# Performance work log

Measured on AMD Instinct MI355X. Metric: run time of the kernel, lower is better.

Reference implementation:

```python
import jax, jax.numpy as jnp
import numpy as np

D_MODEL = 2048
NUM_HEADS = 16
D_K = D_MODEL // NUM_HEADS
THETA = 10000.0
MAX_SEQ_LEN = 2048
GPT_INIT_STD = 0.02


def setup_inputs() -> dict:
    key = jax.random.key(0)
    ks = jax.random.split(key, 5)
    B, T = 4, 2048
    x = jax.random.normal(ks[0], (B, T, D_MODEL), dtype=jnp.float32)
    token_positions = jnp.arange(T, dtype=jnp.int64 if jax.config.jax_enable_x64 else jnp.int32)[None, :]
    Wq = jax.random.normal(ks[1], (D_MODEL, D_MODEL), dtype=jnp.float32) * GPT_INIT_STD
    Wk = jax.random.normal(ks[2], (D_MODEL, D_MODEL), dtype=jnp.float32) * GPT_INIT_STD
    Wv = jax.random.normal(ks[3], (D_MODEL, D_MODEL), dtype=jnp.float32) * GPT_INIT_STD
    Wo = jax.random.normal(ks[4], (D_MODEL, D_MODEL), dtype=jnp.float32) * GPT_INIT_STD
    return {"x": x, "token_positions": token_positions, "Wq": Wq, "Wk": Wk, "Wv": Wv, "Wo": Wo}


def _rope_tables(dtype):
    # angles[p, j] = p * theta^(-2j/d_k), j in [0, d_k/2)
    j = jnp.arange(D_K // 2, dtype=jnp.float32)
    inv_freq = THETA ** (-2.0 * j / float(D_K))
    pos = jnp.arange(MAX_SEQ_LEN, dtype=jnp.float32)[:, None]
    angles = pos * inv_freq[None, :]
    return jnp.cos(angles).astype(dtype), jnp.sin(angles).astype(dtype)


def _apply_rope(t, cos_pos, sin_pos):
    # t: (b, h, s, d); cos/sin: (1, s, d/2) -> broadcast over (b, h)
    even = t[..., 0::2]
    odd = t[..., 1::2]
    c = cos_pos[:, None, :, :]  # (1,1,s,d/2)
    s = sin_pos[:, None, :, :]
    rot_even = even * c - odd * s
    rot_odd = even * s + odd * c
    out = jnp.stack([rot_even, rot_odd], axis=-1)  # (b,h,s,d/2,2)
    return out.reshape(t.shape)


def reference(x, token_positions, Wq, Wk, Wv, Wo):
    B, T, D = x.shape
    H, d = NUM_HEADS, D_K
    q = (x @ Wq.T).reshape(B, T, H, d).transpose(0, 2, 1, 3)  # (b,h,t,d)
    k = (x @ Wk.T).reshape(B, T, H, d).transpose(0, 2, 1, 3)
    v = (x @ Wv.T).reshape(B, T, H, d).transpose(0, 2, 1, 3)

    cos_tab, sin_tab = _rope_tables(x.dtype)
    cos_pos = cos_tab[token_positions]  # (1, t, d/2)
    sin_pos = sin_tab[token_positions]
    q = _apply_rope(q, cos_pos, sin_pos)
    k = _apply_rope(k, cos_pos, sin_pos)

    # token_positions is strictly increasing and attention_mask is None,
    # so build_attention_mask returns None -> unmasked eager attention.
    scale = float(d) ** -0.5
    scores = jnp.einsum('bhtd,bhsd->bhts', q, k) * scale
    attn = jax.nn.softmax(scores.astype(jnp.float32), axis=-1).astype(q.dtype)
    out = jnp.einsum('bhts,bhsd->bhtd', attn, v)  # (b,h,t,d)
    out = out.transpose(0, 2, 1, 3).reshape(B, T, D)  # (b,t,h*d)
    return out @ Wo.T
```

## Files before the change

kernel.cpp:

```cpp
#include <hip/hip_runtime.h>
#include <hip/hip_bf16.h>
#include <math.h>

#define TSEQ   2048
#define DMODEL 2048
#define NHEAD  16
#define DHEAD  128
#define NBATCH 4
#define MROWS  (NBATCH*TSEQ)

typedef __attribute__((ext_vector_type(8))) short v8s;
typedef __attribute__((ext_vector_type(4))) short v4s;
typedef __attribute__((ext_vector_type(4))) float v4f;
typedef __attribute__((ext_vector_type(16))) float v16f;

__device__ __forceinline__ unsigned short f2b(float f) {
  __hip_bfloat16 h = __float2bfloat16(f);
  return *reinterpret_cast<unsigned short*>(&h);
}
__device__ __forceinline__ float b2f(unsigned int u) {
  unsigned short us = (unsigned short)u;
  __hip_bfloat16 h = *reinterpret_cast<__hip_bfloat16*>(&us);
  return __bfloat162float(h);
}
__device__ __forceinline__ unsigned int cvtpk(float lo, float hi) {
  unsigned int r;
  asm("v_cvt_pk_bf16_f32 %0, %1, %2" : "=v"(r) : "v"(lo), "v"(hi));
  return r;
}
__device__ __forceinline__ void gload_lds16(const unsigned short* g, unsigned short* l) {
  __builtin_amdgcn_global_load_lds(
      (const __attribute__((address_space(1))) unsigned int*)g,
      (__attribute__((address_space(3))) unsigned int*)l, 16, 0, 0);
}

__global__ void cvt_f32_to_bf16(const float* __restrict__ in,
                                unsigned short* __restrict__ out, int n4) {
  int i = blockIdx.x * blockDim.x + threadIdx.x;
  if (i >= n4) return;
  float4 v = reinterpret_cast<const float4*>(in)[i];
  ushort4 o;
  o.x = f2b(v.x); o.y = f2b(v.y); o.z = f2b(v.z); o.w = f2b(v.w);
  reinterpret_cast<ushort4*>(out)[i] = o;
}

__global__ void rope_table_kernel(const int* __restrict__ pos,
                                  float* __restrict__ cosT,
                                  float* __restrict__ sinT) {
  int idx = blockIdx.x * blockDim.x + threadIdx.x;
  int t = idx >> 6, j = idx & 63;
  float p = (float)pos[t];
  float inv_freq = expf((-2.0f * (float)j / 128.0f) * logf(10000.0f));
  float ang = p * inv_freq;
  cosT[idx] = cosf(ang);
  sinT[idx] = sinf(ang);
}

template<int MODE>
__global__ __launch_bounds__(512, 2) void gemm8(const unsigned short* __restrict__ A,
                                                const unsigned short* __restrict__ Bt,
                                                void* __restrict__ Cout,
                                                const float* __restrict__ cosT,
                                                const float* __restrict__ sinT) {
  __shared__ unsigned short ldsA[2][256 * 64];
  __shared__ unsigned short ldsB[2][256 * 64];
  const int tid = threadIdx.x;
  const int lane = tid & 63, wv = tid >> 6;
  const int wr = wv >> 2, wc = wv & 3;
  const int g = lane >> 4, r16 = lane & 15;
  const int r7 = r16 & 7;
  const int sl0 = (g ^ r7) << 3;
  const int sl1 = ((4 + g) ^ r7) << 3;

  const int nx = gridDim.x;
  const int nwg = nx * gridDim.y;
  const int lid = blockIdx.y * nx + blockIdx.x;
  const int q8 = nwg >> 3, r8 = nwg & 7;
  const int xcd = lid & 7, off = lid >> 3;
  const int nlid = (xcd < r8 ? xcd * (q8 + 1) : r8 * (q8 + 1) + (xcd - r8) * q8) + off;
  const int mrow0 = (nlid / nx) * 256;
  const int ncol0 = (nlid % nx) * 256;

  const int srow = tid >> 3;
  const int sslot = tid & 7;

  auto stA = [&](int kt, int b, int hf) {
    const int k0 = kt * 64;
#pragma unroll
    for (int j = 0; j < 2; ++j) {
      int r = hf * 128 + j * 64 + srow;
      int slot = sslot ^ (r & 7);
      gload_lds16(&A[(size_t)(mrow0 + r) * DMODEL + k0 + slot * 8],
                  &ldsA[b][(hf * 128 + j * 64) * 64 + tid * 8]);
    }
  };
  auto stB = [&](int kt, int b, int hf) {
    const int k0 = kt * 64;
#pragma unroll
    for (int j = 0; j < 2; ++j) {
      int r = hf * 128 + j * 64 + srow;
      int slot = sslot ^ (r & 7);
      gload_lds16(&Bt[(size_t)(ncol0 + r) * DMODEL + k0 + slot * 8],
                  &ldsB[b][(hf * 128 + j * 64) * 64 + tid * 8]);
    }
  };

  v4f zero = {0.f, 0.f, 0.f, 0.f};
  v4f acc[8][4];
#pragma unroll
  for (int m = 0; m < 8; ++m)
#pragma unroll
    for (int n = 0; n < 4; ++n) acc[m][n] = zero;

  stA(0, 0, 0); stA(0, 0, 1); stB(0, 0, 0); stB(0, 0, 1);
  stA(1, 1, 0); stA(1, 1, 1); stB(1, 1, 0); stB(1, 1, 1);
  asm volatile("s_waitcnt vmcnt(8)" ::: "memory");
  __builtin_amdgcn_s_barrier();

  v8s af[4][2], bf[4][2];
  const int arow = wr * 128 + r16;
  const int brow = wc * 64 + r16;

  for (int kt = 0; kt < DMODEL / 64; ++kt) {
    const int p = kt & 1;
    unsigned short* LA = ldsA[p];
    unsigned short* LB = ldsB[p];

#pragma unroll
    for (int m = 0; m < 4; ++m) {
      af[m][0] = *(const v8s*)&LA[(arow + m * 16) * 64 + sl0];
      af[m][1] = *(const v8s*)&LA[(arow + m * 16) * 64 + sl1];
    }
#pragma unroll
    for (int n = 0; n < 2; ++n) {
      bf[n][0] = *(const v8s*)&LB[(brow + n * 16) * 64 + sl0];
      bf[n][1] = *(const v8s*)&LB[(brow + n * 16) * 64 + sl1];
    }
    __builtin_amdgcn_s_barrier();
    asm volatile("s_waitcnt lgkmcnt(0)" ::: "memory");
    __builtin_amdgcn_sched_barrier(0);
    __builtin_amdgcn_s_setprio(1);
#pragma unroll
    for (int m = 0; m < 4; ++m)
#pragma unroll
      for (int n = 0; n < 2; ++n) {
        acc[m][n] = __builtin_amdgcn_mfma_f32_16x16x32_bf16(af[m][0], bf[n][0], acc[m][n], 0, 0, 0);
        acc[m][n] = __builtin_amdgcn_mfma_f32_16x16x32_bf16(af[m][1], bf[n][1], acc[m][n], 0, 0, 0);
      }
    __builtin_amdgcn_s_setprio(0);
    __builtin_amdgcn_s_barrier();

#pragma unroll
    for (int n = 2; n < 4; ++n) {
      bf[n][0] = *(const v8s*)&LB[(brow + n * 16) * 64 + sl0];
      bf[n][1] = *(const v8s*)&LB[(brow + n * 16) * 64 + sl1];
    }
    __builtin_amdgcn_s_barrier();
    asm volatile("s_waitcnt lgkmcnt(0)" ::: "memory");
    __builtin_amdgcn_sched_barrier(0);
    __builtin_amdgcn_s_setprio(1);
#pragma unroll
    for (int m = 0; m < 4; ++m)
#pragma unroll
      for (int n = 2; n < 4; ++n) {
        acc[m][n] = __builtin_amdgcn_mfma_f32_16x16x32_bf16(af[m][0], bf[n][0], acc[m][n], 0, 0, 0);
        acc[m][n] = __builtin_amdgcn_mfma_f32_16x16x32_bf16(af[m][1], bf[n][1], acc[m][n], 0, 0, 0);
      }
    __builtin_amdgcn_s_setprio(0);
    __builtin_amdgcn_s_barrier();

#pragma unroll
    for (int m = 0; m < 4; ++m) {
      af[m][0] = *(const v8s*)&LA[(arow + 64 + m * 16) * 64 + sl0];
      af[m][1] = *(const v8s*)&LA[(arow + 64 + m * 16) * 64 + sl1];
    }
    if (kt < DMODEL / 64 - 2) { stB(kt + 2, p, 0); stB(kt + 2, p, 1); }
    __builtin_amdgcn_s_barrier();
    asm volatile("s_waitcnt lgkmcnt(0)" ::: "memory");
    __builtin_amdgcn_sched_barrier(0);
    __builtin_amdgcn_s_setprio(1);
#pragma unroll
    for (int m = 0; m < 4; ++m)
#pragma unroll
      for (int n = 2; n < 4; ++n) {
        acc[m + 4][n] = __builtin_amdgcn_mfma_f32_16x16x32_bf16(af[m][0], bf[n][0], acc[m + 4][n], 0, 0, 0);
        acc[m + 4][n] = __builtin_amdgcn_mfma_f32_16x16x32_bf16(af[m][1], bf[n][1], acc[m + 4][n], 0, 0, 0);
      }
    __builtin_amdgcn_s_setprio(0);
    __builtin_amdgcn_s_barrier();

    if (kt < DMODEL / 64 - 2) {
      stA(kt + 2, p, 0); stA(kt + 2, p, 1);
      asm volatile("s_waitcnt vmcnt(8)" ::: "memory");
    } else {
      asm volatile("s_waitcnt vmcnt(0)" ::: "memory");
    }
    __builtin_amdgcn_s_barrier();
    __builtin_amdgcn_s_setprio(1);
#pragma unroll
    for (int m = 0; m < 4; ++m)
#pragma unroll
      for (int n = 0; n < 2; ++n) {
        acc[m + 4][n] = __builtin_amdgcn_mfma_f32_16x16x32_bf16(af[m][0], bf[n][0], acc[m + 4][n], 0, 0, 0);
        acc[m + 4][n] = __builtin_amdgcn_mfma_f32_16x16x32_bf16(af[m][1], bf[n][1], acc[m + 4][n], 0, 0, 0);
      }
    __builtin_amdgcn_s_setprio(0);
    __builtin_amdgcn_s_barrier();
  }

#pragma unroll
  for (int m = 0; m < 8; ++m) {
#pragma unroll
    for (int n = 0; n < 4; ++n) {
#pragma unroll
      for (int r = 0; r < 4; ++r) {
        int row = mrow0 + wr * 128 + m * 16 + g * 4 + r;
        int col = ncol0 + wc * 64 + n * 16 + r16;
        float val = acc[m][n][r];
        if (MODE <= 1) {
          int t = row & (TSEQ - 1), bb = row >> 11;
          int hh = col >> 7, dd = col & (DHEAD - 1);
          float c = cosT[(t << 6) + (dd >> 1)];
          float s = sinT[(t << 6) + (dd >> 1)];
          float pv = __shfl_xor(val, 1);
          float rot = (r16 & 1) ? (pv * s + val * c) : (val * c - pv * s);
          if (MODE == 0) rot *= 0.12751879f;
          ((unsigned short*)Cout)[(((size_t)bb * NHEAD + hh) * TSEQ + t) * DHEAD + dd] = f2b(rot);
        } else if (MODE == 2) {
          int hh = row >> 7, dd = row & (DHEAD - 1);
          int bb = col >> 11, tt = col & (TSEQ - 1);
          ((unsigned short*)Cout)[(((size_t)bb * NHEAD + hh) * DHEAD + dd) * TSEQ + tt] = f2b(val);
        } else {
          ((float*)Cout)[(size_t)row * DMODEL + col] = val;
        }
      }
    }
  }
}

__global__ __launch_bounds__(256, 2) void attn_kernel(const unsigned short* __restrict__ Q,
                                                      const unsigned short* __restrict__ K,
                                                      const unsigned short* __restrict__ Vt,
                                                      unsigned short* __restrict__ O) {
  __shared__ unsigned short Ks[64 * 128];
  __shared__ unsigned short Vs[128 * 64];
  const int tid = threadIdx.x, lane = tid & 63, w = tid >> 6;
  const int hi = lane >> 5, l31 = lane & 31;
  const int bh = blockIdx.y;
  const int b = bh >> 4, h = bh & 15;
  const int qbase = blockIdx.x * 128;
  const size_t hb = (size_t)bh * TSEQ * DHEAD;
  const size_t vb = (size_t)bh * DHEAD * TSEQ;

  v8s qf[8];
  {
    const int qrow = qbase + w * 32 + l31;
#pragma unroll
    for (int dk = 0; dk < 8; ++dk)
      qf[dk] = *(const v8s*)&Q[hb + (size_t)qrow * DHEAD + dk * 16 + hi * 8];
  }

  v16f Z16 = {0,0,0,0,0,0,0,0,0,0,0,0,0,0,0,0};
  v16f o_acc[4];
#pragma unroll
  for (int d = 0; d < 4; ++d) o_acc[d] = Z16;
  float m_run = -1e30f, l_run = 0.0f;

  v8s kst[4], vst[4];
#pragma unroll
  for (int hh = 0; hh < 4; ++hh) {
    int ck = tid + hh * 256;
    kst[hh] = *(const v8s*)&K[hb + (size_t)(ck >> 4) * DHEAD + (ck & 15) * 8];
    vst[hh] = *(const v8s*)&Vt[vb + (size_t)(ck >> 3) * TSEQ + (ck & 7) * 8];
  }
#pragma unroll
  for (int hh = 0; hh < 4; ++hh) {
    int ck = tid + hh * 256;
    int kr = ck >> 4, kc = (ck & 15) * 8;
    *(v8s*)&Ks[kr * 128 + (kc ^ ((kr & 15) << 3))] = kst[hh];
    int vr = ck >> 3, vc = (ck & 7) * 8;
    int g0 = (((vc >> 2)    ) ^ (vr & 15)) << 2;
    int g1 = (((vc >> 2) + 1) ^ (vr & 15)) << 2;
    union { v8s v; v4s hf[2]; } uu; uu.v = vst[hh];
    *(v4s*)&Vs[vr * 64 + g0] = uu.hf[0];
    *(v4s*)&Vs[vr * 64 + g1] = uu.hf[1];
  }
  __syncthreads();

  for (int s0 = 0; s0 < TSEQ; s0 += 64) {
    const bool last = (s0 + 64 >= TSEQ);
    if (!last) {
#pragma unroll
      for (int hh = 0; hh < 4; ++hh) {
        int ck = tid + hh * 256;
        kst[hh] = *(const v8s*)&K[hb + (size_t)(s0 + 64 + (ck >> 4)) * DHEAD + (ck & 15) * 8];
        vst[hh] = *(const v8s*)&Vt[vb + (size_t)(ck >> 3) * TSEQ + s0 + 64 + (ck & 7) * 8];
      }
    }

    v16f s[2]; s[0] = Z16; s[1] = Z16;
    __builtin_amdgcn_s_setprio(1);
#pragma unroll
    for (int kvt = 0; kvt < 2; ++kvt) {
#pragma unroll
      for (int dk = 0; dk < 8; ++dk) {
        int krow = kvt * 32 + l31;
        v8s a = *(const v8s*)&Ks[krow * 128 + ((dk * 16 + hi * 8) ^ ((krow & 15) << 3))];
        s[kvt] = __builtin_amdgcn_mfma_f32_32x32x16_bf16(a, qf[dk], s[kvt], 0, 0, 0);
      }
    }
    __builtin_amdgcn_s_setprio(0);

    float t0[8], t1[4];
#pragma unroll
    for (int i = 0; i < 8; ++i)
      t0[i] = fmaxf(fmaxf(s[0][2*i], s[0][2*i+1]), fmaxf(s[1][2*i], s[1][2*i+1]));
#pragma unroll
    for (int i = 0; i < 4; ++i) t1[i] = fmaxf(t0[2*i], t0[2*i+1]);
    float pm = fmaxf(fmaxf(t1[0], t1[1]), fmaxf(t1[2], t1[3]));
    pm = fmaxf(pm, __shfl_xor(pm, 32));
    if (__any(pm > m_run + 8.0f)) {
      float mnew = fmaxf(m_run, pm);
      float corr = exp2f(m_run - mnew);
      m_run = mnew; l_run *= corr;
#pragma unroll
      for (int r = 0; r < 16; ++r) {
        float cr = __shfl(corr, (r & 3) + 8 * (r >> 2) + 4 * hi);
#pragma unroll
        for (int d = 0; d < 4; ++d) o_acc[d][r] *= cr;
      }
    }
    float rowsum = 0.f;
#pragma unroll
    for (int kvt = 0; kvt < 2; ++kvt)
#pragma unroll
      for (int r = 0; r < 16; ++r) {
        float pp = exp2f(s[kvt][r] - m_run);
        s[kvt][r] = pp; rowsum += pp;
      }
    l_run += rowsum + __shfl_xor(rowsum, 32);

#pragma unroll
    for (int kvt = 0; kvt < 2; ++kvt) {
      unsigned int wpk[8], xw[8];
#pragma unroll
      for (int i = 0; i < 8; ++i) wpk[i] = cvtpk(s[kvt][2 * i], s[kvt][2 * i + 1]);
#pragma unroll
      for (int i = 0; i < 8; ++i) xw[i] = __shfl_xor(wpk[i], 32);
      union { unsigned int u[4]; v8s v; } pa, pb;
      pa.u[0] = hi ? xw[2]  : wpk[0];
      pa.u[1] = hi ? xw[3]  : wpk[1];
      pa.u[2] = hi ? wpk[2] : xw[0];
      pa.u[3] = hi ? wpk[3] : xw[1];
      pb.u[0] = hi ? xw[6]  : wpk[4];
      pb.u[1] = hi ? xw[7]  : wpk[5];
      pb.u[2] = hi ? wpk[6] : xw[4];
      pb.u[3] = hi ? wpk[7] : xw[5];

      const int c0 = kvt * 32 + hi * 8;
      __builtin_amdgcn_s_setprio(1);
#pragma unroll
      for (int d = 0; d < 4; ++d) {
        int drow = d * 32 + l31;
        int sw = (drow & 15) << 2;
        union { v4s hf[2]; v8s v; } vf0, vf1;
        vf0.hf[0] = *(const v4s*)&Vs[drow * 64 + ((c0     ) ^ sw)];
        vf0.hf[1] = *(const v4s*)&Vs[drow * 64 + ((c0 +  4) ^ sw)];
        vf1.hf[0] = *(const v4s*)&Vs[drow * 64 + ((c0 + 16) ^ sw)];
        vf1.hf[1] = *(const v4s*)&Vs[drow * 64 + ((c0 + 20) ^ sw)];
        o_acc[d] = __builtin_amdgcn_mfma_f32_32x32x16_bf16(pa.v, vf0.v, o_acc[d], 0, 0, 0);
        o_acc[d] = __builtin_amdgcn_mfma_f32_32x32x16_bf16(pb.v, vf1.v, o_acc[d], 0, 0, 0);
      }
      __builtin_amdgcn_s_setprio(0);
    }

    __syncthreads();
    if (!last) {
#pragma unroll
      for (int hh = 0; hh < 4; ++hh) {
        int ck = tid + hh * 256;
        int kr = ck >> 4, kc = (ck & 15) * 8;
        *(v8s*)&Ks[kr * 128 + (kc ^ ((kr & 15) << 3))] = kst[hh];
        int vr = ck >> 3, vc = (ck & 7) * 8;
        int g0 = (((vc >> 2)    ) ^ (vr & 15)) << 2;
        int g1 = (((vc >> 2) + 1) ^ (vr & 15)) << 2;
        union { v8s v; v4s hf[2]; } uu; uu.v = vst[hh];
        *(v4s*)&Vs[vr * 64 + g0] = uu.hf[0];
        *(v4s*)&Vs[vr * 64 + g1] = uu.hf[1];
      }
      __syncthreads();
    }
  }

#pragma unroll
  for (int r = 0; r < 16; ++r) {
    int qi = (r & 3) + 8 * (r >> 2) + 4 * hi;
    float lq = __shfl(l_run, qi);
    float inv = 1.0f / lq;
    int t = qbase + w * 32 + qi;
#pragma unroll
    for (int d = 0; d < 4; ++d) {
      O[((size_t)(b * TSEQ + t)) * DMODEL + h * DHEAD + d * 32 + l31] = f2b(o_acc[d][r] * inv);
    }
  }
}

extern "C" void kernel_launch(void* const* d_in, const int* in_sizes, int n_in,
                              void* d_out, int out_size, void* d_ws, size_t ws_size,
                              hipStream_t stream) {
  const float* x  = (const float*)d_in[0];
  const int*   pos = (const int*)d_in[1];
  const float* Wq = (const float*)d_in[2];
  const float* Wk = (const float*)d_in[3];
  const float* Wv = (const float*)d_in[4];
  const float* Wo = (const float*)d_in[5];
  float* out = (float*)d_out;
  char* ws = (char*)d_ws;

  const size_t WBYTES = (size_t)DMODEL * DMODEL * 2;
  const size_t XBYTES = (size_t)MROWS * DMODEL * 2;
  unsigned short* wqb = (unsigned short*)(ws);
  unsigned short* wkb = (unsigned short*)(ws + WBYTES);
  unsigned short* wvb = (unsigned short*)(ws + 2 * WBYTES);
  unsigned short* wob = (unsigned short*)(ws + 3 * WBYTES);
  unsigned short* xb  = (unsigned short*)(ws + 4 * WBYTES);
  unsigned short* Qb  = (unsigned short*)(ws + 4 * WBYTES + XBYTES);
  unsigned short* Kb  = (unsigned short*)(ws + 4 * WBYTES + 2 * XBYTES);
  unsigned short* Vtb = (unsigned short*)(ws + 4 * WBYTES + 3 * XBYTES);
  float* cosT = (float*)(ws + 4 * WBYTES + 4 * XBYTES);
  float* sinT = cosT + TSEQ * 64;
  if (ws_size < 4 * WBYTES + 4 * XBYTES + 2 * (size_t)TSEQ * 64 * sizeof(float)) return;

  cvt_f32_to_bf16<<<(MROWS * DMODEL / 4) / 256, 256, 0, stream>>>(x, xb, MROWS * DMODEL / 4);
  cvt_f32_to_bf16<<<(DMODEL * DMODEL / 4) / 256, 256, 0, stream>>>(Wq, wqb, DMODEL * DMODEL / 4);
  cvt_f32_to_bf16<<<(DMODEL * DMODEL / 4) / 256, 256, 0, stream>>>(Wk, wkb, DMODEL * DMODEL / 4);
  cvt_f32_to_bf16<<<(DMODEL * DMODEL / 4) / 256, 256, 0, stream>>>(Wv, wvb, DMODEL * DMODEL / 4);
  cvt_f32_to_bf16<<<(DMODEL * DMODEL / 4) / 256, 256, 0, stream>>>(Wo, wob, DMODEL * DMODEL / 4);
  rope_table_kernel<<<(TSEQ * 64) / 256, 256, 0, stream>>>(pos, cosT, sinT);

  dim3 gqk(DMODEL / 256, MROWS / 256);
  gemm8<0><<<gqk, 512, 0, stream>>>(xb, wqb, (void*)Qb, cosT, sinT);
  gemm8<1><<<gqk, 512, 0, stream>>>(xb, wkb, (void*)Kb, cosT, sinT);
  gemm8<2><<<dim3(MROWS / 256, DMODEL / 256), 512, 0, stream>>>(wvb, xb, (void*)Vtb, cosT, sinT);

  attn_kernel<<<dim3(TSEQ / 128, 64), 256, 0, stream>>>(Qb, Kb, Vtb, xb);

  gemm8<3><<<gqk, 512, 0, stream>>>(xb, wob, (void*)out, cosT, sinT);
}
```

Before: 551.2 us.

## Fuse prep kernels, merge Q/K GEMMs, use permlane32 swap and native exp2

Replaces five conversion launches and the RoPE table launch with one prep kernel. Merges the Q and K projections into a single GEMM with doubled N; this relies on wkb sitting right after wqb in the workspace so the K weights read as extra rows. Replaces the shfl_xor exchange of packed P values in attention with v_permlane32_swap and uses the hardware exp2 builtin. Together these cut launch overhead, give the GEMM more tiles and trim shuffle and exp cost, at the price of more complex indexing and reliance on the buffer layout.

```diff
diff --git a/kernel.cpp b/kernel.cpp
--- a/kernel.cpp
+++ b/kernel.cpp
@@ -14,14 +14,15 @@
 typedef __attribute__((ext_vector_type(4))) float v4f;
 typedef __attribute__((ext_vector_type(16))) float v16f;
 
+#if __has_builtin(__builtin_amdgcn_exp2f)
+#define EXP2(x) __builtin_amdgcn_exp2f(x)
+#else
+#define EXP2(x) __expf((x) * 0.6931471805599453f)
+#endif
+
 __device__ __forceinline__ unsigned short f2b(float f) {
   __hip_bfloat16 h = __float2bfloat16(f);
   return *reinterpret_cast<unsigned short*>(&h);
-}
-__device__ __forceinline__ float b2f(unsigned int u) {
-  unsigned short us = (unsigned short)u;
-  __hip_bfloat16 h = *reinterpret_cast<__hip_bfloat16*>(&us);
-  return __bfloat162float(h);
 }
 __device__ __forceinline__ unsigned int cvtpk(float lo, float hi) {
   unsigned int r;
@@ -34,32 +35,42 @@
       (__attribute__((address_space(3))) unsigned int*)l, 16, 0, 0);
 }
 
-__global__ void cvt_f32_to_bf16(const float* __restrict__ in,
-                                unsigned short* __restrict__ out, int n4) {
-  int i = blockIdx.x * blockDim.x + threadIdx.x;
-  if (i >= n4) return;
-  float4 v = reinterpret_cast<const float4*>(in)[i];
-  ushort4 o;
-  o.x = f2b(v.x); o.y = f2b(v.y); o.z = f2b(v.z); o.w = f2b(v.w);
-  reinterpret_cast<ushort4*>(out)[i] = o;
-}
-
-__global__ void rope_table_kernel(const int* __restrict__ pos,
-                                  float* __restrict__ cosT,
-                                  float* __restrict__ sinT) {
-  int idx = blockIdx.x * blockDim.x + threadIdx.x;
-  int t = idx >> 6, j = idx & 63;
-  float p = (float)pos[t];
-  float inv_freq = expf((-2.0f * (float)j / 128.0f) * logf(10000.0f));
-  float ang = p * inv_freq;
-  cosT[idx] = cosf(ang);
-  sinT[idx] = sinf(ang);
+__global__ void prep_kernel(const float* __restrict__ x,  const float* __restrict__ Wq,
+                            const float* __restrict__ Wk, const float* __restrict__ Wv,
+                            const float* __restrict__ Wo, const int* __restrict__ pos,
+                            unsigned short* __restrict__ xb,  unsigned short* __restrict__ wqb,
+                            unsigned short* __restrict__ wkb, unsigned short* __restrict__ wvb,
+                            unsigned short* __restrict__ wob,
+                            float* __restrict__ cosT, float* __restrict__ sinT) {
+  const int blk = blockIdx.x, tid = threadIdx.x;
+  if (blk < 32768) {
+    const float* in; unsigned short* out; int lb;
+    if      (blk < 16384) { in = x;  out = xb;  lb = blk; }
+    else if (blk < 20480) { in = Wq; out = wqb; lb = blk - 16384; }
+    else if (blk < 24576) { in = Wk; out = wkb; lb = blk - 20480; }
+    else if (blk < 28672) { in = Wv; out = wvb; lb = blk - 24576; }
+    else                  { in = Wo; out = wob; lb = blk - 28672; }
+    int i = lb * 256 + tid;
+    float4 v = reinterpret_cast<const float4*>(in)[i];
+    ushort4 o;
+    o.x = f2b(v.x); o.y = f2b(v.y); o.z = f2b(v.z); o.w = f2b(v.w);
+    reinterpret_cast<ushort4*>(out)[i] = o;
+  } else {
+    int idx = (blk - 32768) * 256 + tid;
+    int t = idx >> 6, j = idx & 63;
+    float p = (float)pos[t];
+    float inv_freq = expf((-2.0f * (float)j / 128.0f) * logf(10000.0f));
+    float ang = p * inv_freq;
+    cosT[idx] = cosf(ang);
+    sinT[idx] = sinf(ang);
+  }
 }
 
 template<int MODE>
 __global__ __launch_bounds__(512, 2) void gemm8(const unsigned short* __restrict__ A,
                                                 const unsigned short* __restrict__ Bt,
                                                 void* __restrict__ Cout,
+                                                void* __restrict__ CoutK,
                                                 const float* __restrict__ cosT,
                                                 const float* __restrict__ sinT) {
   __shared__ unsigned short ldsA[2][256 * 64];
@@ -217,15 +228,17 @@
         int row = mrow0 + wr * 128 + m * 16 + g * 4 + r;
         int col = ncol0 + wc * 64 + n * 16 + r16;
         float val = acc[m][n][r];
-        if (MODE <= 1) {
+        if (MODE == 0) {
           int t = row & (TSEQ - 1), bb = row >> 11;
-          int hh = col >> 7, dd = col & (DHEAD - 1);
+          int isK = col >> 11;
+          int hh = (col >> 7) & (NHEAD - 1), dd = col & (DHEAD - 1);
           float c = cosT[(t << 6) + (dd >> 1)];
           float s = sinT[(t << 6) + (dd >> 1)];
           float pv = __shfl_xor(val, 1);
           float rot = (r16 & 1) ? (pv * s + val * c) : (val * c - pv * s);
-          if (MODE == 0) rot *= 0.12751879f;
-          ((unsigned short*)Cout)[(((size_t)bb * NHEAD + hh) * TSEQ + t) * DHEAD + dd] = f2b(rot);
+          if (!isK) rot *= 0.12751726f;
+          unsigned short* dst = (unsigned short*)(isK ? CoutK : Cout);
+          dst[(((size_t)bb * NHEAD + hh) * TSEQ + t) * DHEAD + dd] = f2b(rot);
         } else if (MODE == 2) {
           int hh = row >> 7, dd = row & (DHEAD - 1);
           int bb = col >> 11, tt = col & (TSEQ - 1);
@@ -321,7 +334,7 @@
     pm = fmaxf(pm, __shfl_xor(pm, 32));
     if (__any(pm > m_run + 8.0f)) {
       float mnew = fmaxf(m_run, pm);
-      float corr = exp2f(m_run - mnew);
+      float corr = EXP2(m_run - mnew);
       m_run = mnew; l_run *= corr;
 #pragma unroll
       for (int r = 0; r < 16; ++r) {
@@ -335,27 +348,23 @@
     for (int kvt = 0; kvt < 2; ++kvt)
 #pragma unroll
       for (int r = 0; r < 16; ++r) {
-        float pp = exp2f(s[kvt][r] - m_run);
+        float pp = EXP2(s[kvt][r] - m_run);
         s[kvt][r] = pp; rowsum += pp;
       }
     l_run += rowsum + __shfl_xor(rowsum, 32);
 
 #pragma unroll
     for (int kvt = 0; kvt < 2; ++kvt) {
-      unsigned int wpk[8], xw[8];
+      unsigned int wpk[8];
 #pragma unroll
       for (int i = 0; i < 8; ++i) wpk[i] = cvtpk(s[kvt][2 * i], s[kvt][2 * i + 1]);
-#pragma unroll
-      for (int i = 0; i < 8; ++i) xw[i] = __shfl_xor(wpk[i], 32);
+      asm("v_permlane32_swap_b32 %0, %1" : "+v"(wpk[0]), "+v"(wpk[2]));
+      asm("v_permlane32_swap_b32 %0, %1" : "+v"(wpk[1]), "+v"(wpk[3]));
+      asm("v_permlane32_swap_b32 %0, %1" : "+v"(wpk[4]), "+v"(wpk[6]));
+      asm("v_permlane32_swap_b32 %0, %1" : "+v"(wpk[5]), "+v"(wpk[7]));
       union { unsigned int u[4]; v8s v; } pa, pb;
-      pa.u[0] = hi ? xw[2]  : wpk[0];
-      pa.u[1] = hi ? xw[3]  : wpk[1];
-      pa.u[2] = hi ? wpk[2] : xw[0];
-      pa.u[3] = hi ? wpk[3] : xw[1];
-      pb.u[0] = hi ? xw[6]  : wpk[4];
-      pb.u[1] = hi ? xw[7]  : wpk[5];
-      pb.u[2] = hi ? wpk[6] : xw[4];
-      pb.u[3] = hi ? wpk[7] : xw[5];
+      pa.u[0] = wpk[0]; pa.u[1] = wpk[1]; pa.u[2] = wpk[2]; pa.u[3] = wpk[3];
+      pb.u[0] = wpk[4]; pb.u[1] = wpk[5]; pb.u[2] = wpk[6]; pb.u[3] = wpk[7];
 
       const int c0 = kvt * 32 + hi * 8;
       __builtin_amdgcn_s_setprio(1);
@@ -431,19 +440,16 @@
   float* sinT = cosT + TSEQ * 64;
   if (ws_size < 4 * WBYTES + 4 * XBYTES + 2 * (size_t)TSEQ * 64 * sizeof(float)) return;
 
-  cvt_f32_to_bf16<<<(MROWS * DMODEL / 4) / 256, 256, 0, stream>>>(x, xb, MROWS * DMODEL / 4);
-  cvt_f32_to_bf16<<<(DMODEL * DMODEL / 4) / 256, 256, 0, stream>>>(Wq, wqb, DMODEL * DMODEL / 4);
-  cvt_f32_to_bf16<<<(DMODEL * DMODEL / 4) / 256, 256, 0, stream>>>(Wk, wkb, DMODEL * DMODEL / 4);
-  cvt_f32_to_bf16<<<(DMODEL * DMODEL / 4) / 256, 256, 0, stream>>>(Wv, wvb, DMODEL * DMODEL / 4);
-  cvt_f32_to_bf16<<<(DMODEL * DMODEL / 4) / 256, 256, 0, stream>>>(Wo, wob, DMODEL * DMODEL / 4);
-  rope_table_kernel<<<(TSEQ * 64) / 256, 256, 0, stream>>>(pos, cosT, sinT);
-
-  dim3 gqk(DMODEL / 256, MROWS / 256);
-  gemm8<0><<<gqk, 512, 0, stream>>>(xb, wqb, (void*)Qb, cosT, sinT);
-  gemm8<1><<<gqk, 512, 0, stream>>>(xb, wkb, (void*)Kb, cosT, sinT);
-  gemm8<2><<<dim3(MROWS / 256, DMODEL / 256), 512, 0, stream>>>(wvb, xb, (void*)Vtb, cosT, sinT);
+  prep_kernel<<<33280, 256, 0, stream>>>(x, Wq, Wk, Wv, Wo, pos,
+                                         xb, wqb, wkb, wvb, wob, cosT, sinT);
+
+  gemm8<0><<<dim3(2 * DMODEL / 256, MROWS / 256), 512, 0, stream>>>(
+      xb, wqb, (void*)Qb, (void*)Kb, cosT, sinT);
+  gemm8<2><<<dim3(MROWS / 256, DMODEL / 256), 512, 0, stream>>>(
+      wvb, xb, (void*)Vtb, nullptr, cosT, sinT);
 
   attn_kernel<<<dim3(TSEQ / 128, 64), 256, 0, stream>>>(Qb, Kb, Vtb, xb);
 
-  gemm8<3><<<gqk, 512, 0, stream>>>(xb, wob, (void*)out, cosT, sinT);
-}
+  gemm8<3><<<dim3(DMODEL / 256, MROWS / 256), 512, 0, stream>>>(
+      xb, wob, (void*)out, nullptr, cosT, sinT);
+}
```

New measurement: 512.4 us. 7.0% less time.
